# Optimization experiments

Measured on AMD Instinct MI355X. Metric: run time of the kernel, lower is better.

Reference implementation:

```python
import jax, jax.numpy as jnp
import numpy as np

D_MODEL = 1024
N_HEADS = 16
D_K = D_MODEL // N_HEADS


def setup_inputs() -> dict:
    key = jax.random.key(0)
    ks = jax.random.split(key, 5)
    x = jax.random.normal(ks[0], (4, 2048, D_MODEL), dtype=jnp.float32)
    # nn.Linear stores weight as [out, in]; we store transposed [in, out] for x @ W
    w_qkv = jax.random.normal(ks[1], (D_MODEL, 3 * D_MODEL), dtype=jnp.float32) / np.sqrt(D_MODEL)
    b_qkv = jnp.zeros((3 * D_MODEL,), dtype=jnp.float32)
    w_fc = jax.random.normal(ks[2], (D_MODEL, D_MODEL), dtype=jnp.float32) / np.sqrt(D_MODEL)
    b_fc = jnp.zeros((D_MODEL,), dtype=jnp.float32)
    ln_g = jnp.ones((D_MODEL,), dtype=jnp.float32)
    ln_b = jnp.zeros((D_MODEL,), dtype=jnp.float32)
    return {"x": x, "w_qkv": w_qkv, "b_qkv": b_qkv, "w_fc": w_fc, "b_fc": b_fc,
            "ln_g": ln_g, "ln_b": ln_b}


def _layernorm(x, g, b, eps=1e-5):
    mu = jnp.mean(x, axis=-1, keepdims=True)
    var = jnp.mean(jnp.square(x - mu), axis=-1, keepdims=True)
    return (x - mu) * jax.lax.rsqrt(var + eps) * g + b


def reference(x, w_qkv, b_qkv, w_fc, b_fc, ln_g, ln_b):
    residual = x
    xn = _layernorm(x, ln_g, ln_b)
    B, L, D = xn.shape
    qkv = xn @ w_qkv + b_qkv  # [B, L, 3D]
    q, k, v = jnp.split(qkv, 3, axis=-1)
    # b l (h d) -> b h l d
    def to_heads(t):
        return t.reshape(B, L, N_HEADS, D_K).transpose(0, 2, 1, 3)
    q, k, v = to_heads(q), to_heads(k), to_heads(v)
    scale = 1.0 / np.sqrt(D_K)
    scores = jnp.einsum('bhld,bhmd->bhlm', q, k) * scale  # [B,H,L,L]
    attn = jax.nn.softmax(scores, axis=-1)
    # dropout is identity in eval mode
    out = jnp.einsum('bhlm,bhmd->bhld', attn, v)  # [B,H,L,d]
    out = out.transpose(0, 2, 1, 3).reshape(B, L, D)  # b h l d -> b l (h d)
    out = out @ w_fc + b_fc
    return out + residual
```

## Files before the change

### kernel.cpp

```cpp
#include <hip/hip_runtime.h>
#include <hip/hip_bf16.h>
#include <cstdint>
#include <cstddef>

using bf16 = __hip_bfloat16;
typedef __attribute__((ext_vector_type(4))) float f32x4;
typedef __attribute__((ext_vector_type(8))) short bf16x8;

#define D_MODEL 1024
#define SEQ     2048
#define NB      4
#define NHEAD   16
#define DHEAD   64
#define NROWS   (NB * SEQ)

__device__ __forceinline__ void load_lds16(const void* g, void* l) {
  __builtin_amdgcn_global_load_lds(
      (const __attribute__((address_space(1))) unsigned int*)g,
      (__attribute__((address_space(3))) unsigned int*)l, 16, 0, 0);
}

__device__ __forceinline__ unsigned short f2bf(float f) {
  bf16 h = __float2bfloat16(f);
  return *(unsigned short*)&h;
}

__device__ __forceinline__ unsigned pk_trunc(float a, float b) {
  union { float f; unsigned u; } ca, cb;
  ca.f = a; cb.f = b;
  return (ca.u >> 16) | (cb.u & 0xffff0000u);
}

__global__ __launch_bounds__(256) void ln_kernel(
    const float* __restrict__ x, const float* __restrict__ g,
    const float* __restrict__ bb, bf16* __restrict__ xn) {
  int row  = blockIdx.x * 4 + (threadIdx.x >> 6);
  int lane = threadIdx.x & 63;
  const float4* xr = (const float4*)(x + (size_t)row * D_MODEL);
  float v[16], s = 0.f;
#pragma unroll
  for (int i = 0; i < 4; i++) {
    float4 t = xr[lane + 64 * i];
    v[4 * i] = t.x; v[4 * i + 1] = t.y; v[4 * i + 2] = t.z; v[4 * i + 3] = t.w;
    s += t.x + t.y + t.z + t.w;
  }
#pragma unroll
  for (int off = 32; off; off >>= 1) s += __shfl_xor(s, off, 64);
  float mean = s * (1.f / D_MODEL);
  float vs = 0.f;
#pragma unroll
  for (int i = 0; i < 16; i++) { float d = v[i] - mean; vs += d * d; }
#pragma unroll
  for (int off = 32; off; off >>= 1) vs += __shfl_xor(vs, off, 64);
  float rstd = rsqrtf(vs * (1.f / D_MODEL) + 1e-5f);
  ushort4* op = (ushort4*)(xn + (size_t)row * D_MODEL);
#pragma unroll
  for (int i = 0; i < 4; i++) {
    float4 gv = ((const float4*)g)[lane + 64 * i];
    float4 bv = ((const float4*)bb)[lane + 64 * i];
    ushort4 o;
    o.x = f2bf((v[4 * i]     - mean) * rstd * gv.x + bv.x);
    o.y = f2bf((v[4 * i + 1] - mean) * rstd * gv.y + bv.y);
    o.z = f2bf((v[4 * i + 2] - mean) * rstd * gv.z + bv.z);
    o.w = f2bf((v[4 * i + 3] - mean) * rstd * gv.w + bv.w);
    op[lane + 64 * i] = o;
  }
}

__global__ __launch_bounds__(256) void transpose_kernel(
    const float* __restrict__ in, bf16* __restrict__ out, int R, int C) {
  __shared__ float tile[32][33];
  int c0 = blockIdx.x * 32, r0 = blockIdx.y * 32;
  int tx = threadIdx.x & 31, ty = threadIdx.x >> 5;
  for (int i = ty; i < 32; i += 8)
    tile[i][tx] = in[(size_t)(r0 + i) * C + c0 + tx];
  __syncthreads();
  for (int i = ty; i < 32; i += 8)
    out[(size_t)(c0 + i) * R + r0 + tx] = __float2bfloat16(tile[tx][i]);
}

__device__ __forceinline__ void store_ct(bf16* p, float v)  { *p = __float2bfloat16(v); }
__device__ __forceinline__ void store_ct(float* p, float v) { *p = v; }

template <int SPLIT, int RESID, typename CT>
__global__ __launch_bounds__(256) void gemm_bt(
    const bf16* __restrict__ A, const bf16* __restrict__ Bt,
    const float* __restrict__ bias, const float* __restrict__ resid,
    CT* __restrict__ C, bf16* __restrict__ vt, int M, int N, int K) {
  __shared__ __attribute__((aligned(16))) bf16 Alds[128 * 32];
  __shared__ __attribute__((aligned(16))) bf16 Blds[128 * 32];
  int tid = threadIdx.x, wave = tid >> 6, lane = tid & 63;
  int ntiles = N >> 7;
  int bm = blockIdx.x / ntiles, bn = blockIdx.x % ntiles;
  int m0 = bm << 7, n0 = bn << 7;
  int wm = (wave >> 1) << 6, wn = (wave & 1) << 6;
  int srow = tid >> 2, scol = (tid & 3) * 8;
  int frow = lane & 15, fk = (lane >> 4) * 8;
  const bf16* Ap  = A  + (size_t)(m0 + srow) * K + scol;
  const bf16* Ap2 = A  + (size_t)(m0 + 64 + srow) * K + scol;
  const bf16* Bp  = Bt + (size_t)(n0 + srow) * K + scol;
  const bf16* Bp2 = Bt + (size_t)(n0 + 64 + srow) * K + scol;
  f32x4 acc[4][4] = {};
  for (int k0 = 0; k0 < K; k0 += 32) {
    __syncthreads();
    load_lds16(Ap,  (char*)Alds + tid * 16);
    load_lds16(Ap2, (char*)Alds + 4096 + tid * 16);
    load_lds16(Bp,  (char*)Blds + tid * 16);
    load_lds16(Bp2, (char*)Blds + 4096 + tid * 16);
    Ap += 32; Ap2 += 32; Bp += 32; Bp2 += 32;
    __syncthreads();
    bf16x8 af[4], bv[4];
#pragma unroll
    for (int i = 0; i < 4; i++)
      af[i] = *(const bf16x8*)&Alds[(wm + i * 16 + frow) * 32 + fk];
#pragma unroll
    for (int j = 0; j < 4; j++)
      bv[j] = *(const bf16x8*)&Blds[(wn + j * 16 + frow) * 32 + fk];
#pragma unroll
    for (int i = 0; i < 4; i++)
#pragma unroll
      for (int j = 0; j < 4; j++)
        acc[i][j] = __builtin_amdgcn_mfma_f32_16x16x32_bf16(af[i], bv[j], acc[i][j], 0, 0, 0);
  }
#pragma unroll
  for (int i = 0; i < 4; i++) {
    int row0 = m0 + wm + i * 16 + ((lane >> 4) << 2);
#pragma unroll
    for (int j = 0; j < 4; j++) {
      int col = n0 + wn + j * 16 + (lane & 15);
      float bvs = bias[col];
      if (SPLIT && col >= 2048) {
        int hd = col - 2048;
        int b = row0 >> 11, seq0 = row0 & 2047;
        ushort4 pk;
        pk.x = f2bf(acc[i][j][0] + bvs);
        pk.y = f2bf(acc[i][j][1] + bvs);
        pk.z = f2bf(acc[i][j][2] + bvs);
        pk.w = f2bf(acc[i][j][3] + bvs);
        *(ushort4*)&vt[((size_t)(b * 1024 + hd)) * SEQ + seq0] = pk;
      } else {
        int stride = SPLIT ? 2048 : N;
        float scale = (SPLIT && col < 1024) ? 0.18033688f : 1.0f;
#pragma unroll
        for (int r = 0; r < 4; r++) {
          size_t idx = (size_t)(row0 + r) * stride + col;
          float val = (acc[i][j][r] + bvs) * scale;
          if (RESID) val += resid[idx];
          store_ct(&C[idx], val);
        }
      }
    }
  }
}

__global__ __launch_bounds__(256) void attn_kernel(
    const bf16* __restrict__ qk, const bf16* __restrict__ vt,
    bf16* __restrict__ aout) {
  int bh = blockIdx.x;
  int qt = blockIdx.y;
  int bb = bh >> 4, h = bh & 15;
  const bf16* Qg = qk + (size_t)bb * SEQ * 2048 + h * DHEAD;
  const bf16* Kg = Qg + D_MODEL;
  const bf16* Vg = vt + (size_t)bh * DHEAD * SEQ;

  __shared__ __attribute__((aligned(16))) bf16 Qlds[128 * 64];
  __shared__ __attribute__((aligned(16))) bf16 Klds[64 * 64];
  __shared__ __attribute__((aligned(16))) bf16 Vlds[64 * 64];
  __shared__ __attribute__((aligned(16))) bf16 Plds[4 * 32 * 72];

  int tid = threadIdx.x, wave = tid >> 6, lane = tid & 63;
  int prow = tid >> 3, pch = tid & 7;
  int lch8 = ((pch ^ (prow & 7)) << 3);
  int frow = lane & 15, quad = lane >> 4;
  int e0 = ((quad ^ (frow & 7)) << 3);
  int q0 = qt * 128;
  bf16* Pw = Plds + wave * 32 * 72;

#pragma unroll
  for (int s2 = 0; s2 < 4; s2++)
    load_lds16(Qg + (size_t)(q0 + s2 * 32 + prow) * 2048 + lch8,
               (char*)Qlds + s2 * 4096 + tid * 16);
  __syncthreads();
  bf16x8 qf[2][2];
#pragma unroll
  for (int qtile = 0; qtile < 2; qtile++)
#pragma unroll
    for (int kk = 0; kk < 2; kk++)
      qf[qtile][kk] =
          *(const bf16x8*)&Qlds[(wave * 32 + qtile * 16 + frow) * 64 + (e0 ^ (kk * 32))];

  f32x4 l4[2] = {};
  f32x4 o[4][2] = {};

  for (int kt = 0; kt < SEQ / 64; kt++) {
    int kv0 = kt * 64;
    __syncthreads();
#pragma unroll
    for (int s2 = 0; s2 < 2; s2++) {
      load_lds16(Kg + (size_t)(kv0 + s2 * 32 + prow) * 2048 + lch8,
                 (char*)Klds + s2 * 4096 + tid * 16);
      load_lds16(Vg + (size_t)(s2 * 32 + prow) * SEQ + kv0 + lch8,
                 (char*)Vlds + s2 * 4096 + tid * 16);
    }
    __syncthreads();

    f32x4 s[4][2] = {};
#pragma unroll
    for (int mt = 0; mt < 4; mt++) {
      bf16x8 af0 = *(const bf16x8*)&Klds[(mt * 16 + frow) * 64 + e0];
      bf16x8 af1 = *(const bf16x8*)&Klds[(mt * 16 + frow) * 64 + (e0 ^ 32)];
#pragma unroll
      for (int qtile = 0; qtile < 2; qtile++) {
        s[mt][qtile] = __builtin_amdgcn_mfma_f32_16x16x32_bf16(af0, qf[qtile][0], s[mt][qtile], 0, 0, 0);
        s[mt][qtile] = __builtin_amdgcn_mfma_f32_16x16x32_bf16(af1, qf[qtile][1], s[mt][qtile], 0, 0, 0);
      }
    }

#pragma unroll
    for (int qtile = 0; qtile < 2; qtile++)
#pragma unroll
      for (int mt = 0; mt < 4; mt++) {
        f32x4 pv;
        pv[0] = __builtin_amdgcn_exp2f(s[mt][qtile][0]);
        pv[1] = __builtin_amdgcn_exp2f(s[mt][qtile][1]);
        pv[2] = __builtin_amdgcn_exp2f(s[mt][qtile][2]);
        pv[3] = __builtin_amdgcn_exp2f(s[mt][qtile][3]);
        l4[qtile] += pv;
        uint2 pk2;
        pk2.x = pk_trunc(pv[0], pv[1]);
        pk2.y = pk_trunc(pv[2], pv[3]);
        *(uint2*)&Pw[(qtile * 16 + frow) * 72 + mt * 16 + quad * 4] = pk2;
      }

    bf16x8 pf[2][2];
#pragma unroll
    for (int qtile = 0; qtile < 2; qtile++)
#pragma unroll
      for (int kk = 0; kk < 2; kk++)
        pf[qtile][kk] = *(const bf16x8*)&Pw[(qtile * 16 + frow) * 72 + kk * 32 + quad * 8];
#pragma unroll
    for (int dt = 0; dt < 4; dt++) {
      bf16x8 vf0 = *(const bf16x8*)&Vlds[(dt * 16 + frow) * 64 + e0];
      bf16x8 vf1 = *(const bf16x8*)&Vlds[(dt * 16 + frow) * 64 + (e0 ^ 32)];
#pragma unroll
      for (int qtile = 0; qtile < 2; qtile++) {
        o[dt][qtile] = __builtin_amdgcn_mfma_f32_16x16x32_bf16(vf0, pf[qtile][0], o[dt][qtile], 0, 0, 0);
        o[dt][qtile] = __builtin_amdgcn_mfma_f32_16x16x32_bf16(vf1, pf[qtile][1], o[dt][qtile], 0, 0, 0);
      }
    }
  }

  float linv[2];
#pragma unroll
  for (int qtile = 0; qtile < 2; qtile++) {
    float v = (l4[qtile][0] + l4[qtile][1]) + (l4[qtile][2] + l4[qtile][3]);
    v += __shfl_xor(v, 16, 64);
    v += __shfl_xor(v, 32, 64);
    linv[qtile] = 1.f / v;
  }

#pragma unroll
  for (int qtile = 0; qtile < 2; qtile++)
#pragma unroll
    for (int dt = 0; dt < 4; dt++) {
      ushort4 pk;
      pk.x = f2bf(o[dt][qtile][0] * linv[qtile]);
      pk.y = f2bf(o[dt][qtile][1] * linv[qtile]);
      pk.z = f2bf(o[dt][qtile][2] * linv[qtile]);
      pk.w = f2bf(o[dt][qtile][3] * linv[qtile]);
      *(ushort4*)&Pw[(qtile * 16 + frow) * 72 + dt * 16 + quad * 4] = pk;
    }
  int rq = lane >> 1, d0 = (lane & 1) * 32;
  size_t grow = (size_t)(bb * SEQ + q0 + wave * 32 + rq);
#pragma unroll
  for (int i = 0; i < 4; i++) {
    bf16x8 v8 = *(const bf16x8*)&Pw[rq * 72 + d0 + i * 8];
    *(bf16x8*)&aout[grow * D_MODEL + h * DHEAD + d0 + i * 8] = v8;
  }
}

extern "C" void kernel_launch(void* const* d_in, const int* in_sizes, int n_in,
                              void* d_out, int out_size, void* d_ws, size_t ws_size,
                              hipStream_t stream) {
  const float* x     = (const float*)d_in[0];
  const float* w_qkv = (const float*)d_in[1];
  const float* b_qkv = (const float*)d_in[2];
  const float* w_fc  = (const float*)d_in[3];
  const float* b_fc  = (const float*)d_in[4];
  const float* ln_g  = (const float*)d_in[5];
  const float* ln_b  = (const float*)d_in[6];
  float* out = (float*)d_out;

  char* ws = (char*)d_ws;
  bf16* xn    = (bf16*)(ws);
  bf16* wqkvT = (bf16*)(ws + (16u << 20));
  bf16* wfcT  = (bf16*)(ws + (22u << 20));
  bf16* qk    = (bf16*)(ws + (24u << 20));
  bf16* vt    = (bf16*)(ws + (56u << 20));
  bf16* aout  = (bf16*)(ws);

  ln_kernel<<<NROWS / 4, 256, 0, stream>>>(x, ln_g, ln_b, xn);
  transpose_kernel<<<dim3(3 * D_MODEL / 32, D_MODEL / 32), 256, 0, stream>>>(
      w_qkv, wqkvT, D_MODEL, 3 * D_MODEL);
  transpose_kernel<<<dim3(D_MODEL / 32, D_MODEL / 32), 256, 0, stream>>>(
      w_fc, wfcT, D_MODEL, D_MODEL);
  gemm_bt<1, 0, bf16><<<(NROWS / 128) * (3 * D_MODEL / 128), 256, 0, stream>>>(
      xn, wqkvT, b_qkv, nullptr, qk, vt, NROWS, 3 * D_MODEL, D_MODEL);
  attn_kernel<<<dim3(NB * NHEAD, SEQ / 128), 256, 0, stream>>>(qk, vt, aout);
  gemm_bt<0, 1, float><<<(NROWS / 128) * (D_MODEL / 128), 256, 0, stream>>>(
      aout, wfcT, b_fc, x, out, nullptr, NROWS, D_MODEL, D_MODEL);
}
```

Baseline: 316.7 us.

## Keep softmax probabilities in registers by permuting V layout in QKV epilogue

The QKV GEMM epilogue now writes the transposed V tensor in a permuted sequence order, so the P fragments produced by the QK^T MFMA line up with the B-operand layout of the PV MFMA. The attention kernel can then pack P straight from registers, dropping the per-iteration LDS round trip and the dedicated P buffer. The output staging reuses the Q/K/V LDS after a barrier. Launch bounds now request 4 blocks per SM to use the freed LDS for occupancy, which risks register pressure or spills.

```diff
diff --git a/kernel.cpp b/kernel.cpp
--- a/kernel.cpp
+++ b/kernel.cpp
@@ -132,12 +132,14 @@
       if (SPLIT && col >= 2048) {
         int hd = col - 2048;
         int b = row0 >> 11, seq0 = row0 & 2047;
+        int within = seq0 & 63, mt = within >> 4, q4 = (within >> 2) & 3;
+        int pos = (seq0 & ~63) + ((mt >> 1) << 5) + (q4 << 3) + ((mt & 1) << 2);
         ushort4 pk;
         pk.x = f2bf(acc[i][j][0] + bvs);
         pk.y = f2bf(acc[i][j][1] + bvs);
         pk.z = f2bf(acc[i][j][2] + bvs);
         pk.w = f2bf(acc[i][j][3] + bvs);
-        *(ushort4*)&vt[((size_t)(b * 1024 + hd)) * SEQ + seq0] = pk;
+        *(ushort4*)&vt[((size_t)(b * 1024 + hd)) * SEQ + pos] = pk;
       } else {
         int stride = SPLIT ? 2048 : N;
         float scale = (SPLIT && col < 1024) ? 0.18033688f : 1.0f;
@@ -153,7 +155,7 @@
   }
 }
 
-__global__ __launch_bounds__(256) void attn_kernel(
+__global__ __launch_bounds__(256, 4) void attn_kernel(
     const bf16* __restrict__ qk, const bf16* __restrict__ vt,
     bf16* __restrict__ aout) {
   int bh = blockIdx.x;
@@ -166,7 +168,6 @@
   __shared__ __attribute__((aligned(16))) bf16 Qlds[128 * 64];
   __shared__ __attribute__((aligned(16))) bf16 Klds[64 * 64];
   __shared__ __attribute__((aligned(16))) bf16 Vlds[64 * 64];
-  __shared__ __attribute__((aligned(16))) bf16 Plds[4 * 32 * 72];
 
   int tid = threadIdx.x, wave = tid >> 6, lane = tid & 63;
   int prow = tid >> 3, pch = tid & 7;
@@ -174,7 +175,6 @@
   int frow = lane & 15, quad = lane >> 4;
   int e0 = ((quad ^ (frow & 7)) << 3);
   int q0 = qt * 128;
-  bf16* Pw = Plds + wave * 32 * 72;
 
 #pragma unroll
   for (int s2 = 0; s2 < 4; s2++)
@@ -216,6 +216,7 @@
       }
     }
 
+    uint2 pk[2][4];
 #pragma unroll
     for (int qtile = 0; qtile < 2; qtile++)
 #pragma unroll
@@ -226,26 +227,23 @@
         pv[2] = __builtin_amdgcn_exp2f(s[mt][qtile][2]);
         pv[3] = __builtin_amdgcn_exp2f(s[mt][qtile][3]);
         l4[qtile] += pv;
-        uint2 pk2;
-        pk2.x = pk_trunc(pv[0], pv[1]);
-        pk2.y = pk_trunc(pv[2], pv[3]);
-        *(uint2*)&Pw[(qtile * 16 + frow) * 72 + mt * 16 + quad * 4] = pk2;
+        pk[qtile][mt].x = pk_trunc(pv[0], pv[1]);
+        pk[qtile][mt].y = pk_trunc(pv[2], pv[3]);
       }
 
-    bf16x8 pf[2][2];
-#pragma unroll
-    for (int qtile = 0; qtile < 2; qtile++)
-#pragma unroll
-      for (int kk = 0; kk < 2; kk++)
-        pf[qtile][kk] = *(const bf16x8*)&Pw[(qtile * 16 + frow) * 72 + kk * 32 + quad * 8];
 #pragma unroll
     for (int dt = 0; dt < 4; dt++) {
       bf16x8 vf0 = *(const bf16x8*)&Vlds[(dt * 16 + frow) * 64 + e0];
       bf16x8 vf1 = *(const bf16x8*)&Vlds[(dt * 16 + frow) * 64 + (e0 ^ 32)];
 #pragma unroll
       for (int qtile = 0; qtile < 2; qtile++) {
-        o[dt][qtile] = __builtin_amdgcn_mfma_f32_16x16x32_bf16(vf0, pf[qtile][0], o[dt][qtile], 0, 0, 0);
-        o[dt][qtile] = __builtin_amdgcn_mfma_f32_16x16x32_bf16(vf1, pf[qtile][1], o[dt][qtile], 0, 0, 0);
+        union { unsigned u[4]; bf16x8 v; } pf0, pf1;
+        pf0.u[0] = pk[qtile][0].x; pf0.u[1] = pk[qtile][0].y;
+        pf0.u[2] = pk[qtile][1].x; pf0.u[3] = pk[qtile][1].y;
+        pf1.u[0] = pk[qtile][2].x; pf1.u[1] = pk[qtile][2].y;
+        pf1.u[2] = pk[qtile][3].x; pf1.u[3] = pk[qtile][3].y;
+        o[dt][qtile] = __builtin_amdgcn_mfma_f32_16x16x32_bf16(vf0, pf0.v, o[dt][qtile], 0, 0, 0);
+        o[dt][qtile] = __builtin_amdgcn_mfma_f32_16x16x32_bf16(vf1, pf1.v, o[dt][qtile], 0, 0, 0);
       }
     }
   }
@@ -259,6 +257,10 @@
     linv[qtile] = 1.f / v;
   }
 
+  __syncthreads();
+  bf16* Tw = (wave == 0) ? Qlds
+           : (wave == 1) ? Qlds + 32 * 80
+           : (wave == 2) ? Klds : Vlds;
 #pragma unroll
   for (int qtile = 0; qtile < 2; qtile++)
 #pragma unroll
@@ -268,13 +270,13 @@
       pk.y = f2bf(o[dt][qtile][1] * linv[qtile]);
       pk.z = f2bf(o[dt][qtile][2] * linv[qtile]);
       pk.w = f2bf(o[dt][qtile][3] * linv[qtile]);
-      *(ushort4*)&Pw[(qtile * 16 + frow) * 72 + dt * 16 + quad * 4] = pk;
+      *(ushort4*)&Tw[(qtile * 16 + frow) * 80 + dt * 16 + quad * 4] = pk;
     }
   int rq = lane >> 1, d0 = (lane & 1) * 32;
   size_t grow = (size_t)(bb * SEQ + q0 + wave * 32 + rq);
 #pragma unroll
   for (int i = 0; i < 4; i++) {
-    bf16x8 v8 = *(const bf16x8*)&Pw[rq * 72 + d0 + i * 8];
+    bf16x8 v8 = *(const bf16x8*)&Tw[rq * 80 + d0 + i * 8];
     *(bf16x8*)&aout[grow * D_MODEL + h * DHEAD + d0 + i * 8] = v8;
   }
 }
```

Measured after the change: 286.5 us. 1.11x faster.
